# Kernel optimization log

Hardware: AMD Instinct MI355X
Metric: run time of the kernel (lower is better)

## Reference

```python
import jax, jax.numpy as jnp
import numpy as np
from jax import lax

B, T, I, H, L, O = 256, 1024, 64, 128, 2, 1


def setup_inputs() -> dict:
    key = jax.random.key(0)
    ks = jax.random.split(key, 4 * L + 3)
    s = 1.0 / np.sqrt(H)  # PyTorch LSTM init scale
    inp = {"x": jax.random.normal(ks[0], (B, T, I), dtype=jnp.float32)}
    for l in range(L):
        in_dim = I if l == 0 else H
        inp[f"W_ih_{l}"] = jax.random.uniform(ks[1 + 4 * l], (4 * H, in_dim), minval=-s, maxval=s)
        inp[f"W_hh_{l}"] = jax.random.uniform(ks[2 + 4 * l], (4 * H, H), minval=-s, maxval=s)
        inp[f"b_ih_{l}"] = jax.random.uniform(ks[3 + 4 * l], (4 * H,), minval=-s, maxval=s)
        inp[f"b_hh_{l}"] = jax.random.uniform(ks[4 + 4 * l], (4 * H,), minval=-s, maxval=s)
    inp["W_lin"] = jax.random.uniform(ks[-2], (O, H), minval=-s, maxval=s)
    inp["b_lin"] = jax.random.uniform(ks[-1], (O,), minval=-s, maxval=s)
    return inp


def _lstm_layer(x, W_ih, W_hh, b_ih, b_hh):
    # x: [B, T, in] -> hidden states [B, T, H]; PyTorch gate order i, f, g, o
    b = b_ih + b_hh
    # precompute input projections for all timesteps (one big GEMM)
    x_proj = jnp.einsum('bti,gi->btg', x, W_ih) + b  # [B, T, 4H]

    def step(carry, xp_t):
        h, c = carry
        gates = xp_t + h @ W_hh.T  # [B, 4H]
        i, f, g, o = jnp.split(gates, 4, axis=-1)
        c = jax.nn.sigmoid(f) * c + jax.nn.sigmoid(i) * jnp.tanh(g)
        h = jax.nn.sigmoid(o) * jnp.tanh(c)
        return (h, c), h

    h0 = jnp.zeros((x.shape[0], W_hh.shape[1]), x.dtype)
    (_, _), hs = lax.scan(step, (h0, h0), jnp.swapaxes(x_proj, 0, 1))
    return jnp.swapaxes(hs, 0, 1)  # [B, T, H]


def reference(x, W_ih_0, W_hh_0, b_ih_0, b_hh_0, W_ih_1, W_hh_1, b_ih_1, b_hh_1, W_lin, b_lin):
    h = _lstm_layer(x, W_ih_0, W_hh_0, b_ih_0, b_hh_0)
    h = _lstm_layer(h, W_ih_1, W_hh_1, b_ih_1, b_hh_1)
    return h[:, -1] @ W_lin.T + b_lin  # [B, O]
```

## Files before the change

kernel.cpp:

```cpp
#include <hip/hip_runtime.h>


typedef __attribute__((ext_vector_type(4))) float f32x4;
typedef _Float16 f16x8 __attribute__((ext_vector_type(8)));
typedef short s16x8 __attribute__((ext_vector_type(8)));

#define NB    256
#define TSEQ  1024
#define II    64
#define HH    128
#define G4    512
#define TC    16
#define NCH   (TSEQ/TC)
#define SCL   0.0009765625f
#define SCLI  1024.f

#define F_WHH0  0
#define F_WHH1  8192
#define F_WIH1  16384
#define F_WIH0  24576
#define F_TOTAL 28672

#define H0G_OFF   458752ULL
#define H0G_WORDS (256ULL*1024ULL*128ULL)
#define FLAG_OFF  (H0G_OFF + H0G_WORDS*4ULL)
#define WS_NEEDED (FLAG_OFF + 1024ULL)

#define KEEP4I(v) asm volatile("" : "+v"((v).x), "+v"((v).y), "+v"((v).z), "+v"((v).w))

__device__ __forceinline__ float tanh_f(float x){
    float ax = fabsf(x);
    float e  = __expf(2.f*ax);
    float t  = 1.f - 2.f*__builtin_amdgcn_rcpf(e + 1.f);
    return copysignf(t, x);
}
__device__ __forceinline__ f32x4 mfma16(int4 a, f16x8 b, f32x4 c){
    return __builtin_amdgcn_mfma_f32_16x16x32_f16(
        __builtin_bit_cast(f16x8, a), b, c, 0, 0, 0);
}
__device__ __forceinline__ f16x8 ldb(const _Float16* p){
    return __builtin_bit_cast(f16x8, *(const int4*)p);
}
__device__ __forceinline__ void unpack8(int4 v0, int4 v1, f16x8& bh, f16x8& bl){
    s16x8 hb, lb;
    hb[0]=(short)v0.x; lb[0]=(short)(((unsigned)v0.x)>>16);
    hb[1]=(short)v0.y; lb[1]=(short)(((unsigned)v0.y)>>16);
    hb[2]=(short)v0.z; lb[2]=(short)(((unsigned)v0.z)>>16);
    hb[3]=(short)v0.w; lb[3]=(short)(((unsigned)v0.w)>>16);
    hb[4]=(short)v1.x; lb[4]=(short)(((unsigned)v1.x)>>16);
    hb[5]=(short)v1.y; lb[5]=(short)(((unsigned)v1.y)>>16);
    hb[6]=(short)v1.z; lb[6]=(short)(((unsigned)v1.z)>>16);
    hb[7]=(short)v1.w; lb[7]=(short)(((unsigned)v1.w)>>16);
    bh = __builtin_bit_cast(f16x8, hb);
    bl = __builtin_bit_cast(f16x8, lb);
}

__global__ void pack_w(const float* __restrict__ Wih0, const float* __restrict__ Whh0,
                       const float* __restrict__ Wih1, const float* __restrict__ Whh1,
                       int4* __restrict__ ws)
{
    int fid = blockIdx.x * 256 + threadIdx.x;
    if (fid >= F_TOTAL) return;
    const float* src; int nks; int rb;
    if (fid < F_WHH1)      { src = Whh0; nks = 4; rb = fid; }
    else if (fid < F_WIH1) { src = Whh1; nks = 4; rb = fid - F_WHH1; }
    else if (fid < F_WIH0) { src = Wih1; nks = 4; rb = fid - F_WIH1; }
    else                   { src = Wih0; nks = 2; rb = fid - F_WIH0; }
    int lane = rb & 63;
    int rem  = rb >> 6;
    int s    = rem % nks;
    int t    = (rem / nks) & 3;
    int w    = rem / (nks * 4);
    int row  = t * 128 + w * 16 + (lane & 15);
    int K    = nks * 32;
    int k0   = s * 32 + (lane >> 4) * 8;
    const float* p = src + (size_t)row * K + k0;
    unsigned short us[8];
    #pragma unroll
    for (int j = 0; j < 8; ++j)
        us[j] = __builtin_bit_cast(unsigned short, (_Float16)p[j]);
    int4 o;
    o.x = (int)((unsigned)us[0] | ((unsigned)us[1] << 16));
    o.y = (int)((unsigned)us[2] | ((unsigned)us[3] << 16));
    o.z = (int)((unsigned)us[4] | ((unsigned)us[5] << 16));
    o.w = (int)((unsigned)us[6] | ((unsigned)us[7] << 16));
    ws[fid] = o;
}

struct LaneCtx {
    int gsel, usel, u, xpr, base;
    bool writer, is_g, odd;
    int lk;
};

template<bool PING>
__device__ __forceinline__ void serial_steps(
    const LaneCtx& L, const int4 (&Ahi)[4][4],
    float (*xp)[G4],
    _Float16* hh_rd_base, _Float16* hl_rd_base, int rd_stride,
    _Float16* hh_wr_base, _Float16* hl_wr_base, int wr_stride,
    float* h1f, float& c)
{
    #pragma unroll 1
    for (int t = 0; t < TC; ++t){
        int rs = PING ? (t & 1) : t;
        int wsl = PING ? ((t+1) & 1) : (t+1);
        const _Float16* bp = L.odd ? (hl_rd_base + rs*rd_stride)
                                   : (hh_rd_base + rs*rd_stride);
        float xpv = xp[t][L.xpr];
        f32x4 acc[4];
        #pragma unroll
        for (int t4 = 0; t4 < 4; ++t4) acc[t4] = (f32x4){0.f,0.f,0.f,0.f};
        #pragma unroll
        for (int s = 0; s < 4; ++s){
            f16x8 bv = ldb(&bp[s*32 + L.lk*8]);
            #pragma unroll
            for (int t4 = 0; t4 < 4; ++t4) acc[t4] = mfma16(Ahi[t4][s], bv, acc[t4]);
        }
        f32x4 ps;
        {
            f32x4 p01 = (L.gsel & 1) ? acc[1] : acc[0];
            f32x4 p23 = (L.gsel & 1) ? acc[3] : acc[2];
            ps = (L.gsel & 2) ? p23 : p01;
        }
        float own, oth;
        {
            float a01 = (L.usel & 1) ? ps[1] : ps[0];
            float a23 = (L.usel & 1) ? ps[3] : ps[2];
            own = (L.usel & 2) ? a23 : a01;
            float b01 = (L.usel & 1) ? ps[0] : ps[1];
            float b23 = (L.usel & 1) ? ps[2] : ps[3];
            oth = (L.usel & 2) ? b23 : b01;
        }
        float recv = __shfl_xor(oth, 1);
        float pre  = (L.odd ? (recv + SCL*own) : (own + SCL*recv)) + xpv;
        float z    = tanh_f(L.is_g ? pre : 0.5f*pre);
        float y    = L.is_g ? z : 0.5f*z + 0.5f;
        float gi = __shfl(y, L.base);
        float gf = __shfl(y, L.base | 4);
        float gg = __shfl(y, L.base | 8);
        float go = __shfl(y, L.base | 12);
        c = gf*c + gi*gg;
        float h = go * tanh_f(c);
        _Float16 hf = (_Float16)h;
        _Float16 hl = (_Float16)((h - (float)hf) * SCLI);
        if (L.writer){
            (hh_wr_base + wsl*wr_stride)[L.u] = hf;
            (hl_wr_base + wsl*wr_stride)[L.u] = hl;
            if (h1f) h1f[L.u] = h;
        }
        __syncthreads();
    }
}

__global__ __launch_bounds__(512, 2)
void lstm_dual(const float* __restrict__ x,
               const float* __restrict__ bih0, const float* __restrict__ bhh0,
               const float* __restrict__ bih1, const float* __restrict__ bhh1,
               const float* __restrict__ Wlin, const float* __restrict__ blin,
               const int4* __restrict__ ws,
               unsigned* __restrict__ h0g,
               int* __restrict__ prod,
               float* __restrict__ out)
{
    const int tid  = threadIdx.x;
    const int lane = tid & 63;
    const int w    = tid >> 6;
    const int lm   = lane & 15;
    const int lk   = lane >> 4;

    LaneCtx L;
    L.gsel = lm >> 2;  L.usel = lm & 3;  L.lk = lk;
    L.u    = w*16 + lk*4 + L.usel;
    L.xpr  = L.gsel*128 + w*16 + lk*4 + L.usel;
    L.base = lane & 0x33;
    L.writer = (L.gsel == 0);
    L.is_g   = (L.gsel == 2);
    L.odd    = (lane & 1);

    __shared__ __align__(16) char smem[46624];
    float (*xp)[G4] = (float(*)[G4])smem;

    if (blockIdx.x < NB) {
        const int row = blockIdx.x;
        _Float16 (*h0_hi)[136] = (_Float16(*)[136])(smem + 32768);
        _Float16 (*h0_lo)[136] = (_Float16(*)[136])(smem + 37392);
        _Float16 (*xc_hi)[72]  = (_Float16(*)[72]) (smem + 42016);
        _Float16 (*xc_lo)[72]  = (_Float16(*)[72]) (smem + 44320);

        if (tid < HH){ h0_hi[0][tid] = (_Float16)0.f; h0_lo[0][tid] = (_Float16)0.f; }
        float c0 = 0.f;
        const float* xb = x + (size_t)row * TSEQ * II;
        __syncthreads();

        #pragma unroll 1
        for (int ch = 0; ch < NCH; ++ch){
            {
                int i0 = tid, i1 = tid + 512;
                float v0 = xb[(size_t)ch*TC*II + i0];
                float v1 = xb[(size_t)ch*TC*II + i1];
                _Float16 a0 = (_Float16)v0, a1 = (_Float16)v1;
                xc_hi[i0>>6][i0&63] = a0; xc_lo[i0>>6][i0&63] = (_Float16)((v0-(float)a0)*SCLI);
                xc_hi[i1>>6][i1&63] = a1; xc_lo[i1>>6][i1&63] = (_Float16)((v1-(float)a1)*SCLI);
            }
            if (ch > 0 && tid < HH){
                h0_hi[0][tid] = h0_hi[TC][tid];
                h0_lo[0][tid] = h0_lo[TC][tid];
            }
            __syncthreads();

            {
                f32x4 acc[4], accL[4];
                #pragma unroll
                for (int t4 = 0; t4 < 4; ++t4){
                    acc[t4]  = (f32x4){0.f,0.f,0.f,0.f};
                    accL[t4] = (f32x4){0.f,0.f,0.f,0.f};
                }
                #pragma unroll
                for (int s = 0; s < 2; ++s){
                    f16x8 bh = ldb(&xc_hi[lm][s*32 + lk*8]);
                    f16x8 bl = ldb(&xc_lo[lm][s*32 + lk*8]);
                    int4 ah[4];
                    #pragma unroll
                    for (int t4 = 0; t4 < 4; ++t4)
                        ah[t4] = ws[F_WIH0 + (((w*4 + t4)*2 + s) << 6) + lane];
                    #pragma unroll
                    for (int t4 = 0; t4 < 4; ++t4) acc[t4]  = mfma16(ah[t4], bh, acc[t4]);
                    #pragma unroll
                    for (int t4 = 0; t4 < 4; ++t4) accL[t4] = mfma16(ah[t4], bl, accL[t4]);
                }
                #pragma unroll
                for (int t4 = 0; t4 < 4; ++t4){
                    int rowb = t4*128 + w*16 + lk*4;
                    f32x4 bs = *(const f32x4*)(bih0+rowb) + *(const f32x4*)(bhh0+rowb);
                    *(f32x4*)&xp[lm][rowb] = acc[t4] + accL[t4]*SCL + bs;
                }
            }
            __syncthreads();

            int4 Ahi[4][4];
            #pragma unroll
            for (int t4 = 0; t4 < 4; ++t4)
                #pragma unroll
                for (int s = 0; s < 4; ++s)
                    Ahi[t4][s] = ws[F_WHH0 + (((w*4 + t4)*4 + s) << 6) + lane];
            #pragma unroll
            for (int t4 = 0; t4 < 4; ++t4)
                #pragma unroll
                for (int s = 0; s < 4; ++s) KEEP4I(Ahi[t4][s]);

            serial_steps<false>(L, Ahi, xp,
                                &h0_hi[0][0], &h0_lo[0][0], 136,
                                &h0_hi[0][0], &h0_lo[0][0], 136,
                                nullptr, c0);

            {
                size_t gbase = ((size_t)row*TSEQ + (size_t)ch*TC)*HH;
                #pragma unroll
                for (int k = 0; k < 4; ++k){
                    int idx = tid + 512*k;
                    int t = idx >> 7, u = idx & 127;
                    unsigned ph = (unsigned)__builtin_bit_cast(unsigned short, h0_hi[t+1][u]);
                    unsigned pl = (unsigned)__builtin_bit_cast(unsigned short, h0_lo[t+1][u]);
                    h0g[gbase + idx] = ph | (pl << 16);
                }
            }
            __syncthreads();
            if (tid == 0)
                __hip_atomic_store(&prod[row], ch+1, __ATOMIC_RELEASE,
                                   __HIP_MEMORY_SCOPE_AGENT);
        }
    } else {
        const int row = blockIdx.x - NB;
        _Float16 (*h1_hi)[HH] = (_Float16(*)[HH])(smem + 32768);
        _Float16 (*h1_lo)[HH] = (_Float16(*)[HH])(smem + 33280);
        float*    h1f         = (float*)(smem + 33792);

        if (tid < HH){ h1_hi[0][tid] = (_Float16)0.f; h1_lo[0][tid] = (_Float16)0.f;
                       h1f[tid] = 0.f; }
        float c1 = 0.f;
        __syncthreads();

        #pragma unroll 1
        for (int ch = 0; ch < NCH; ++ch){
            {
                int v = __hip_atomic_load(&prod[row], __ATOMIC_RELAXED,
                                          __HIP_MEMORY_SCOPE_AGENT);
                while (v < ch+1){
                    __builtin_amdgcn_s_sleep(8);
                    v = __hip_atomic_load(&prod[row], __ATOMIC_RELAXED,
                                          __HIP_MEMORY_SCOPE_AGENT);
                }
                (void)__hip_atomic_load(&prod[row], __ATOMIC_ACQUIRE,
                                        __HIP_MEMORY_SCOPE_AGENT);
            }
            {
                f32x4 acc[4], accL[4];
                #pragma unroll
                for (int t4 = 0; t4 < 4; ++t4){
                    acc[t4]  = (f32x4){0.f,0.f,0.f,0.f};
                    accL[t4] = (f32x4){0.f,0.f,0.f,0.f};
                }
                size_t gbase = ((size_t)row*TSEQ + (size_t)ch*TC + lm)*HH;
                #pragma unroll
                for (int s = 0; s < 4; ++s){
                    const int4* gp = (const int4*)(h0g + gbase + s*32 + lk*8);
                    int4 v0 = gp[0], v1 = gp[1];
                    f16x8 bh, bl;
                    unpack8(v0, v1, bh, bl);
                    int4 ah[4];
                    #pragma unroll
                    for (int t4 = 0; t4 < 4; ++t4)
                        ah[t4] = ws[F_WIH1 + (((w*4 + t4)*4 + s) << 6) + lane];
                    #pragma unroll
                    for (int t4 = 0; t4 < 4; ++t4) acc[t4]  = mfma16(ah[t4], bh, acc[t4]);
                    #pragma unroll
                    for (int t4 = 0; t4 < 4; ++t4) accL[t4] = mfma16(ah[t4], bl, accL[t4]);
                }
                #pragma unroll
                for (int t4 = 0; t4 < 4; ++t4){
                    int rowb = t4*128 + w*16 + lk*4;
                    f32x4 bs = *(const f32x4*)(bih1+rowb) + *(const f32x4*)(bhh1+rowb);
                    *(f32x4*)&xp[lm][rowb] = acc[t4] + accL[t4]*SCL + bs;
                }
            }
            __syncthreads();

            int4 Ahi[4][4];
            #pragma unroll
            for (int t4 = 0; t4 < 4; ++t4)
                #pragma unroll
                for (int s = 0; s < 4; ++s)
                    Ahi[t4][s] = ws[F_WHH1 + (((w*4 + t4)*4 + s) << 6) + lane];
            #pragma unroll
            for (int t4 = 0; t4 < 4; ++t4)
                #pragma unroll
                for (int s = 0; s < 4; ++s) KEEP4I(Ahi[t4][s]);

            serial_steps<true>(L, Ahi, xp,
                               &h1_hi[0][0], &h1_lo[0][0], HH,
                               &h1_hi[0][0], &h1_lo[0][0], HH,
                               h1f, c1);
        }

        if (tid < 64){
            float s = h1f[tid]*Wlin[tid] + h1f[tid+64]*Wlin[tid+64];
            #pragma unroll
            for (int off = 32; off; off >>= 1) s += __shfl_down(s, off);
            if (tid == 0) out[row] = s + blin[0];
        }
    }
}

extern "C" void kernel_launch(void* const* d_in, const int* in_sizes, int n_in,
                              void* d_out, int out_size, void* d_ws, size_t ws_size,
                              hipStream_t stream)
{
    const float* x    = (const float*)d_in[0];
    const float* Wih0 = (const float*)d_in[1];
    const float* Whh0 = (const float*)d_in[2];
    const float* bih0 = (const float*)d_in[3];
    const float* bhh0 = (const float*)d_in[4];
    const float* Wih1 = (const float*)d_in[5];
    const float* Whh1 = (const float*)d_in[6];
    const float* bih1 = (const float*)d_in[7];
    const float* bhh1 = (const float*)d_in[8];
    const float* Wlin = (const float*)d_in[9];
    const float* blin = (const float*)d_in[10];

    if (ws_size < WS_NEEDED) return;

    char* wsb = (char*)d_ws;
    int4*     ws   = (int4*)wsb;
    unsigned* h0g  = (unsigned*)(wsb + H0G_OFF);
    int*      prod = (int*)(wsb + FLAG_OFF);

    (void)hipMemsetAsync(prod, 0, 1024, stream);
    hipLaunchKernelGGL(pack_w, dim3(F_TOTAL/256), dim3(256), 0, stream,
                       Wih0, Whh0, Wih1, Whh1, ws);
    hipLaunchKernelGGL(lstm_dual, dim3(2*NB), dim3(512), 0, stream,
                       x, bih0, bhh0, bih1, bhh1, Wlin, blin,
                       ws, h0g, prod, (float*)d_out);
}
```

Before: 1.692 ms.

## Fuse both LSTM layers into one 1024-thread block with a skewed chunk pipeline

Replaces the two cooperating 512-thread blocks, which passed layer-0 hidden states through a global buffer guarded by atomic flags, with a single 1024-thread block per batch row. Waves 0-7 run layer 0 on chunk ch while waves 8-15 run layer 1 on chunk ch-1, reading h0 straight from shared memory. This removes the global h0 round trip, the spin-wait polling and the workspace memset. In exchange, every timestep now needs a barrier across all 16 waves. The kernel is forced to 128 VGPRs and one block per CU, which risks register spills and lower occupancy.

```diff
diff --git a/kernel.cpp b/kernel.cpp
--- a/kernel.cpp
+++ b/kernel.cpp
@@ -3,7 +3,6 @@
 
 typedef __attribute__((ext_vector_type(4))) float f32x4;
 typedef _Float16 f16x8 __attribute__((ext_vector_type(8)));
-typedef short s16x8 __attribute__((ext_vector_type(8)));
 
 #define NB    256
 #define TSEQ  1024
@@ -21,11 +20,6 @@
 #define F_WIH0  24576
 #define F_TOTAL 28672
 
-#define H0G_OFF   458752ULL
-#define H0G_WORDS (256ULL*1024ULL*128ULL)
-#define FLAG_OFF  (H0G_OFF + H0G_WORDS*4ULL)
-#define WS_NEEDED (FLAG_OFF + 1024ULL)
-
 #define KEEP4I(v) asm volatile("" : "+v"((v).x), "+v"((v).y), "+v"((v).z), "+v"((v).w))
 
 __device__ __forceinline__ float tanh_f(float x){
@@ -40,19 +34,6 @@
 }
 __device__ __forceinline__ f16x8 ldb(const _Float16* p){
     return __builtin_bit_cast(f16x8, *(const int4*)p);
-}
-__device__ __forceinline__ void unpack8(int4 v0, int4 v1, f16x8& bh, f16x8& bl){
-    s16x8 hb, lb;
-    hb[0]=(short)v0.x; lb[0]=(short)(((unsigned)v0.x)>>16);
-    hb[1]=(short)v0.y; lb[1]=(short)(((unsigned)v0.y)>>16);
-    hb[2]=(short)v0.z; lb[2]=(short)(((unsigned)v0.z)>>16);
-    hb[3]=(short)v0.w; lb[3]=(short)(((unsigned)v0.w)>>16);
-    hb[4]=(short)v1.x; lb[4]=(short)(((unsigned)v1.x)>>16);
-    hb[5]=(short)v1.y; lb[5]=(short)(((unsigned)v1.y)>>16);
-    hb[6]=(short)v1.z; lb[6]=(short)(((unsigned)v1.z)>>16);
-    hb[7]=(short)v1.w; lb[7]=(short)(((unsigned)v1.w)>>16);
-    bh = __builtin_bit_cast(f16x8, hb);
-    bl = __builtin_bit_cast(f16x8, lb);
 }
 
 __global__ void pack_w(const float* __restrict__ Wih0, const float* __restrict__ Whh0,
@@ -93,262 +74,218 @@
     int lk;
 };
 
-template<bool PING>
-__device__ __forceinline__ void serial_steps(
+__device__ __forceinline__ void step_body(
     const LaneCtx& L, const int4 (&Ahi)[4][4],
-    float (*xp)[G4],
-    _Float16* hh_rd_base, _Float16* hl_rd_base, int rd_stride,
-    _Float16* hh_wr_base, _Float16* hl_wr_base, int wr_stride,
+    const float* xpt,
+    const _Float16* hh_rd, const _Float16* hl_rd,
+    _Float16* hh_wr, _Float16* hl_wr,
     float* h1f, float& c)
 {
-    #pragma unroll 1
-    for (int t = 0; t < TC; ++t){
-        int rs = PING ? (t & 1) : t;
-        int wsl = PING ? ((t+1) & 1) : (t+1);
-        const _Float16* bp = L.odd ? (hl_rd_base + rs*rd_stride)
-                                   : (hh_rd_base + rs*rd_stride);
-        float xpv = xp[t][L.xpr];
-        f32x4 acc[4];
+    const _Float16* bp = L.odd ? hl_rd : hh_rd;
+    float xpv = xpt[L.xpr];
+    f32x4 acc[4];
+    #pragma unroll
+    for (int t4 = 0; t4 < 4; ++t4) acc[t4] = (f32x4){0.f,0.f,0.f,0.f};
+    #pragma unroll
+    for (int s = 0; s < 4; ++s){
+        f16x8 bv = ldb(&bp[s*32 + L.lk*8]);
         #pragma unroll
-        for (int t4 = 0; t4 < 4; ++t4) acc[t4] = (f32x4){0.f,0.f,0.f,0.f};
-        #pragma unroll
-        for (int s = 0; s < 4; ++s){
-            f16x8 bv = ldb(&bp[s*32 + L.lk*8]);
-            #pragma unroll
-            for (int t4 = 0; t4 < 4; ++t4) acc[t4] = mfma16(Ahi[t4][s], bv, acc[t4]);
-        }
-        f32x4 ps;
-        {
-            f32x4 p01 = (L.gsel & 1) ? acc[1] : acc[0];
-            f32x4 p23 = (L.gsel & 1) ? acc[3] : acc[2];
-            ps = (L.gsel & 2) ? p23 : p01;
-        }
-        float own, oth;
-        {
-            float a01 = (L.usel & 1) ? ps[1] : ps[0];
-            float a23 = (L.usel & 1) ? ps[3] : ps[2];
-            own = (L.usel & 2) ? a23 : a01;
-            float b01 = (L.usel & 1) ? ps[0] : ps[1];
-            float b23 = (L.usel & 1) ? ps[2] : ps[3];
-            oth = (L.usel & 2) ? b23 : b01;
-        }
-        float recv = __shfl_xor(oth, 1);
-        float pre  = (L.odd ? (recv + SCL*own) : (own + SCL*recv)) + xpv;
-        float z    = tanh_f(L.is_g ? pre : 0.5f*pre);
-        float y    = L.is_g ? z : 0.5f*z + 0.5f;
-        float gi = __shfl(y, L.base);
-        float gf = __shfl(y, L.base | 4);
-        float gg = __shfl(y, L.base | 8);
-        float go = __shfl(y, L.base | 12);
-        c = gf*c + gi*gg;
-        float h = go * tanh_f(c);
-        _Float16 hf = (_Float16)h;
-        _Float16 hl = (_Float16)((h - (float)hf) * SCLI);
-        if (L.writer){
-            (hh_wr_base + wsl*wr_stride)[L.u] = hf;
-            (hl_wr_base + wsl*wr_stride)[L.u] = hl;
-            if (h1f) h1f[L.u] = h;
-        }
-        __syncthreads();
-    }
-}
-
-__global__ __launch_bounds__(512, 2)
-void lstm_dual(const float* __restrict__ x,
-               const float* __restrict__ bih0, const float* __restrict__ bhh0,
-               const float* __restrict__ bih1, const float* __restrict__ bhh1,
-               const float* __restrict__ Wlin, const float* __restrict__ blin,
-               const int4* __restrict__ ws,
-               unsigned* __restrict__ h0g,
-               int* __restrict__ prod,
-               float* __restrict__ out)
+        for (int t4 = 0; t4 < 4; ++t4) acc[t4] = mfma16(Ahi[t4][s], bv, acc[t4]);
+    }
+    f32x4 ps;
+    {
+        f32x4 p01 = (L.gsel & 1) ? acc[1] : acc[0];
+        f32x4 p23 = (L.gsel & 1) ? acc[3] : acc[2];
+        ps = (L.gsel & 2) ? p23 : p01;
+    }
+    float own, oth;
+    {
+        float a01 = (L.usel & 1) ? ps[1] : ps[0];
+        float a23 = (L.usel & 1) ? ps[3] : ps[2];
+        own = (L.usel & 2) ? a23 : a01;
+        float b01 = (L.usel & 1) ? ps[0] : ps[1];
+        float b23 = (L.usel & 1) ? ps[2] : ps[3];
+        oth = (L.usel & 2) ? b23 : b01;
+    }
+    float recv = __shfl_xor(oth, 1);
+    float pre  = (L.odd ? (recv + SCL*own) : (own + SCL*recv)) + xpv;
+    float z    = tanh_f(L.is_g ? pre : 0.5f*pre);
+    float y    = L.is_g ? z : 0.5f*z + 0.5f;
+    float gi = __shfl(y, L.base);
+    float gf = __shfl(y, L.base | 4);
+    float gg = __shfl(y, L.base | 8);
+    float go = __shfl(y, L.base | 12);
+    c = gf*c + gi*gg;
+    float h = go * tanh_f(c);
+    _Float16 hf = (_Float16)h;
+    _Float16 hl = (_Float16)((h - (float)hf) * SCLI);
+    if (L.writer){
+        hh_wr[L.u] = hf;
+        hl_wr[L.u] = hl;
+        if (h1f) h1f[L.u] = h;
+    }
+}
+
+__global__
+__attribute__((amdgpu_flat_work_group_size(1024,1024),
+               amdgpu_waves_per_eu(4,4),
+               amdgpu_num_vgpr(128)))
+void lstm_fused(const float* __restrict__ x,
+                const float* __restrict__ bih0, const float* __restrict__ bhh0,
+                const float* __restrict__ bih1, const float* __restrict__ bhh1,
+                const float* __restrict__ Wlin, const float* __restrict__ blin,
+                const int4* __restrict__ ws,
+                float* __restrict__ out)
 {
+    const int b    = blockIdx.x;
     const int tid  = threadIdx.x;
     const int lane = tid & 63;
     const int w    = tid >> 6;
+    const int eng  = w >> 3;
+    const int we   = w & 7;
     const int lm   = lane & 15;
     const int lk   = lane >> 4;
 
     LaneCtx L;
     L.gsel = lm >> 2;  L.usel = lm & 3;  L.lk = lk;
-    L.u    = w*16 + lk*4 + L.usel;
-    L.xpr  = L.gsel*128 + w*16 + lk*4 + L.usel;
+    L.u    = we*16 + lk*4 + L.usel;
+    L.xpr  = L.gsel*128 + we*16 + lk*4 + L.usel;
     L.base = lane & 0x33;
     L.writer = (L.gsel == 0);
     L.is_g   = (L.gsel == 2);
     L.odd    = (lane & 1);
 
-    __shared__ __align__(16) char smem[46624];
-    float (*xp)[G4] = (float(*)[G4])smem;
-
-    if (blockIdx.x < NB) {
-        const int row = blockIdx.x;
-        _Float16 (*h0_hi)[136] = (_Float16(*)[136])(smem + 32768);
-        _Float16 (*h0_lo)[136] = (_Float16(*)[136])(smem + 37392);
-        _Float16 (*xc_hi)[72]  = (_Float16(*)[72]) (smem + 42016);
-        _Float16 (*xc_lo)[72]  = (_Float16(*)[72]) (smem + 44320);
-
-        if (tid < HH){ h0_hi[0][tid] = (_Float16)0.f; h0_lo[0][tid] = (_Float16)0.f; }
-        float c0 = 0.f;
-        const float* xb = x + (size_t)row * TSEQ * II;
-        __syncthreads();
-
-        #pragma unroll 1
-        for (int ch = 0; ch < NCH; ++ch){
-            {
-                int i0 = tid, i1 = tid + 512;
-                float v0 = xb[(size_t)ch*TC*II + i0];
-                float v1 = xb[(size_t)ch*TC*II + i1];
-                _Float16 a0 = (_Float16)v0, a1 = (_Float16)v1;
-                xc_hi[i0>>6][i0&63] = a0; xc_lo[i0>>6][i0&63] = (_Float16)((v0-(float)a0)*SCLI);
-                xc_hi[i1>>6][i1&63] = a1; xc_lo[i1>>6][i1&63] = (_Float16)((v1-(float)a1)*SCLI);
-            }
+    __shared__ __align__(16) float    xp0[TC][G4];
+    __shared__ __align__(16) float    xp1[TC][G4];
+    __shared__ __align__(16) _Float16 h0_hi[TC+1][136];
+    __shared__ __align__(16) _Float16 h0_lo[TC+1][136];
+    __shared__ __align__(16) _Float16 xc_hi[TC][72];
+    __shared__ __align__(16) _Float16 xc_lo[TC][72];
+    __shared__ __align__(16) _Float16 h1_hi[2][HH];
+    __shared__ __align__(16) _Float16 h1_lo[2][HH];
+    __shared__ __align__(16) float    h1f[HH];
+
+    if (tid < HH){ h0_hi[0][tid] = (_Float16)0.f; h0_lo[0][tid] = (_Float16)0.f; }
+    else if (tid >= 512 && tid < 512 + HH){
+        int u = tid - 512;
+        h1_hi[0][u] = (_Float16)0.f; h1_lo[0][u] = (_Float16)0.f; h1f[u] = 0.f;
+    }
+    float c = 0.f;
+    const float* xb = x + (size_t)b * TSEQ * II;
+    __syncthreads();
+
+    #pragma unroll 1
+    for (int ch = 0; ch <= NCH; ++ch){
+        const bool l0 = (ch < NCH);
+        const bool l1 = (ch > 0);
+
+        if (eng == 0 && l0){
+            int i0 = tid, i1 = tid + 512;
+            float v0 = xb[(size_t)ch*TC*II + i0];
+            float v1 = xb[(size_t)ch*TC*II + i1];
+            _Float16 a0 = (_Float16)v0, a1 = (_Float16)v1;
+            xc_hi[i0>>6][i0&63] = a0; xc_lo[i0>>6][i0&63] = (_Float16)((v0-(float)a0)*SCLI);
+            xc_hi[i1>>6][i1&63] = a1; xc_lo[i1>>6][i1&63] = (_Float16)((v1-(float)a1)*SCLI);
             if (ch > 0 && tid < HH){
                 h0_hi[0][tid] = h0_hi[TC][tid];
                 h0_lo[0][tid] = h0_lo[TC][tid];
             }
+        }
+        __syncthreads();
+
+        if (eng == 0 && l0){
+            f32x4 acc[4], accL[4];
+            #pragma unroll
+            for (int t4 = 0; t4 < 4; ++t4){
+                acc[t4]  = (f32x4){0.f,0.f,0.f,0.f};
+                accL[t4] = (f32x4){0.f,0.f,0.f,0.f};
+            }
+            #pragma unroll
+            for (int s = 0; s < 2; ++s){
+                f16x8 bh = ldb(&xc_hi[lm][s*32 + lk*8]);
+                f16x8 bl = ldb(&xc_lo[lm][s*32 + lk*8]);
+                int4 ah[4];
+                #pragma unroll
+                for (int t4 = 0; t4 < 4; ++t4)
+                    ah[t4] = ws[F_WIH0 + (((we*4 + t4)*2 + s) << 6) + lane];
+                #pragma unroll
+                for (int t4 = 0; t4 < 4; ++t4) acc[t4]  = mfma16(ah[t4], bh, acc[t4]);
+                #pragma unroll
+                for (int t4 = 0; t4 < 4; ++t4) accL[t4] = mfma16(ah[t4], bl, accL[t4]);
+            }
+            #pragma unroll
+            for (int t4 = 0; t4 < 4; ++t4){
+                int rowb = t4*128 + we*16 + lk*4;
+                f32x4 bs = *(const f32x4*)(bih0+rowb) + *(const f32x4*)(bhh0+rowb);
+                *(f32x4*)&xp0[lm][rowb] = acc[t4] + accL[t4]*SCL + bs;
+            }
+        } else if (eng == 1 && l1){
+            f32x4 acc[4], accL[4];
+            #pragma unroll
+            for (int t4 = 0; t4 < 4; ++t4){
+                acc[t4]  = (f32x4){0.f,0.f,0.f,0.f};
+                accL[t4] = (f32x4){0.f,0.f,0.f,0.f};
+            }
+            #pragma unroll
+            for (int s = 0; s < 4; ++s){
+                f16x8 bh = ldb(&h0_hi[lm + 1][s*32 + lk*8]);
+                f16x8 bl = ldb(&h0_lo[lm + 1][s*32 + lk*8]);
+                int4 ah[4];
+                #pragma unroll
+                for (int t4 = 0; t4 < 4; ++t4)
+                    ah[t4] = ws[F_WIH1 + (((we*4 + t4)*4 + s) << 6) + lane];
+                #pragma unroll
+                for (int t4 = 0; t4 < 4; ++t4) acc[t4]  = mfma16(ah[t4], bh, acc[t4]);
+                #pragma unroll
+                for (int t4 = 0; t4 < 4; ++t4) accL[t4] = mfma16(ah[t4], bl, accL[t4]);
+            }
+            #pragma unroll
+            for (int t4 = 0; t4 < 4; ++t4){
+                int rowb = t4*128 + we*16 + lk*4;
+                f32x4 bs = *(const f32x4*)(bih1+rowb) + *(const f32x4*)(bhh1+rowb);
+                *(f32x4*)&xp1[lm][rowb] = acc[t4] + accL[t4]*SCL + bs;
+            }
+        }
+        __syncthreads();
+
+        int4 Ahi[4][4];
+        {
+            const int F = eng ? F_WHH1 : F_WHH0;
+            #pragma unroll
+            for (int t4 = 0; t4 < 4; ++t4)
+                #pragma unroll
+                for (int s = 0; s < 4; ++s)
+                    Ahi[t4][s] = ws[F + (((we*4 + t4)*4 + s) << 6) + lane];
+            #pragma unroll
+            for (int t4 = 0; t4 < 4; ++t4)
+                #pragma unroll
+                for (int s = 0; s < 4; ++s) KEEP4I(Ahi[t4][s]);
+        }
+
+        #pragma unroll 1
+        for (int t = 0; t < TC; ++t){
+            if (eng == 0){
+                if (l0)
+                    step_body(L, Ahi, &xp0[t][0],
+                              &h0_hi[t][0], &h0_lo[t][0],
+                              &h0_hi[t+1][0], &h0_lo[t+1][0],
+                              nullptr, c);
+            } else {
+                if (l1)
+                    step_body(L, Ahi, &xp1[t][0],
+                              &h1_hi[t&1][0], &h1_lo[t&1][0],
+                              &h1_hi[(t+1)&1][0], &h1_lo[(t+1)&1][0],
+                              h1f, c);
+            }
             __syncthreads();
-
-            {
-                f32x4 acc[4], accL[4];
-                #pragma unroll
-                for (int t4 = 0; t4 < 4; ++t4){
-                    acc[t4]  = (f32x4){0.f,0.f,0.f,0.f};
-                    accL[t4] = (f32x4){0.f,0.f,0.f,0.f};
-                }
-                #pragma unroll
-                for (int s = 0; s < 2; ++s){
-                    f16x8 bh = ldb(&xc_hi[lm][s*32 + lk*8]);
-                    f16x8 bl = ldb(&xc_lo[lm][s*32 + lk*8]);
-                    int4 ah[4];
-                    #pragma unroll
-                    for (int t4 = 0; t4 < 4; ++t4)
-                        ah[t4] = ws[F_WIH0 + (((w*4 + t4)*2 + s) << 6) + lane];
-                    #pragma unroll
-                    for (int t4 = 0; t4 < 4; ++t4) acc[t4]  = mfma16(ah[t4], bh, acc[t4]);
-                    #pragma unroll
-                    for (int t4 = 0; t4 < 4; ++t4) accL[t4] = mfma16(ah[t4], bl, accL[t4]);
-                }
-                #pragma unroll
-                for (int t4 = 0; t4 < 4; ++t4){
-                    int rowb = t4*128 + w*16 + lk*4;
-                    f32x4 bs = *(const f32x4*)(bih0+rowb) + *(const f32x4*)(bhh0+rowb);
-                    *(f32x4*)&xp[lm][rowb] = acc[t4] + accL[t4]*SCL + bs;
-                }
-            }
-            __syncthreads();
-
-            int4 Ahi[4][4];
-            #pragma unroll
-            for (int t4 = 0; t4 < 4; ++t4)
-                #pragma unroll
-                for (int s = 0; s < 4; ++s)
-                    Ahi[t4][s] = ws[F_WHH0 + (((w*4 + t4)*4 + s) << 6) + lane];
-            #pragma unroll
-            for (int t4 = 0; t4 < 4; ++t4)
-                #pragma unroll
-                for (int s = 0; s < 4; ++s) KEEP4I(Ahi[t4][s]);
-
-            serial_steps<false>(L, Ahi, xp,
-                                &h0_hi[0][0], &h0_lo[0][0], 136,
-                                &h0_hi[0][0], &h0_lo[0][0], 136,
-                                nullptr, c0);
-
-            {
-                size_t gbase = ((size_t)row*TSEQ + (size_t)ch*TC)*HH;
-                #pragma unroll
-                for (int k = 0; k < 4; ++k){
-                    int idx = tid + 512*k;
-                    int t = idx >> 7, u = idx & 127;
-                    unsigned ph = (unsigned)__builtin_bit_cast(unsigned short, h0_hi[t+1][u]);
-                    unsigned pl = (unsigned)__builtin_bit_cast(unsigned short, h0_lo[t+1][u]);
-                    h0g[gbase + idx] = ph | (pl << 16);
-                }
-            }
-            __syncthreads();
-            if (tid == 0)
-                __hip_atomic_store(&prod[row], ch+1, __ATOMIC_RELEASE,
-                                   __HIP_MEMORY_SCOPE_AGENT);
         }
-    } else {
-        const int row = blockIdx.x - NB;
-        _Float16 (*h1_hi)[HH] = (_Float16(*)[HH])(smem + 32768);
-        _Float16 (*h1_lo)[HH] = (_Float16(*)[HH])(smem + 33280);
-        float*    h1f         = (float*)(smem + 33792);
-
-        if (tid < HH){ h1_hi[0][tid] = (_Float16)0.f; h1_lo[0][tid] = (_Float16)0.f;
-                       h1f[tid] = 0.f; }
-        float c1 = 0.f;
-        __syncthreads();
-
-        #pragma unroll 1
-        for (int ch = 0; ch < NCH; ++ch){
-            {
-                int v = __hip_atomic_load(&prod[row], __ATOMIC_RELAXED,
-                                          __HIP_MEMORY_SCOPE_AGENT);
-                while (v < ch+1){
-                    __builtin_amdgcn_s_sleep(8);
-                    v = __hip_atomic_load(&prod[row], __ATOMIC_RELAXED,
-                                          __HIP_MEMORY_SCOPE_AGENT);
-                }
-                (void)__hip_atomic_load(&prod[row], __ATOMIC_ACQUIRE,
-                                        __HIP_MEMORY_SCOPE_AGENT);
-            }
-            {
-                f32x4 acc[4], accL[4];
-                #pragma unroll
-                for (int t4 = 0; t4 < 4; ++t4){
-                    acc[t4]  = (f32x4){0.f,0.f,0.f,0.f};
-                    accL[t4] = (f32x4){0.f,0.f,0.f,0.f};
-                }
-                size_t gbase = ((size_t)row*TSEQ + (size_t)ch*TC + lm)*HH;
-                #pragma unroll
-                for (int s = 0; s < 4; ++s){
-                    const int4* gp = (const int4*)(h0g + gbase + s*32 + lk*8);
-                    int4 v0 = gp[0], v1 = gp[1];
-                    f16x8 bh, bl;
-                    unpack8(v0, v1, bh, bl);
-                    int4 ah[4];
-                    #pragma unroll
-                    for (int t4 = 0; t4 < 4; ++t4)
-                        ah[t4] = ws[F_WIH1 + (((w*4 + t4)*4 + s) << 6) + lane];
-                    #pragma unroll
-                    for (int t4 = 0; t4 < 4; ++t4) acc[t4]  = mfma16(ah[t4], bh, acc[t4]);
-                    #pragma unroll
-                    for (int t4 = 0; t4 < 4; ++t4) accL[t4] = mfma16(ah[t4], bl, accL[t4]);
-                }
-                #pragma unroll
-                for (int t4 = 0; t4 < 4; ++t4){
-                    int rowb = t4*128 + w*16 + lk*4;
-                    f32x4 bs = *(const f32x4*)(bih1+rowb) + *(const f32x4*)(bhh1+rowb);
-                    *(f32x4*)&xp[lm][rowb] = acc[t4] + accL[t4]*SCL + bs;
-                }
-            }
-            __syncthreads();
-
-            int4 Ahi[4][4];
-            #pragma unroll
-            for (int t4 = 0; t4 < 4; ++t4)
-                #pragma unroll
-                for (int s = 0; s < 4; ++s)
-                    Ahi[t4][s] = ws[F_WHH1 + (((w*4 + t4)*4 + s) << 6) + lane];
-            #pragma unroll
-            for (int t4 = 0; t4 < 4; ++t4)
-                #pragma unroll
-                for (int s = 0; s < 4; ++s) KEEP4I(Ahi[t4][s]);
-
-            serial_steps<true>(L, Ahi, xp,
-                               &h1_hi[0][0], &h1_lo[0][0], HH,
-                               &h1_hi[0][0], &h1_lo[0][0], HH,
-                               h1f, c1);
-        }
-
-        if (tid < 64){
-            float s = h1f[tid]*Wlin[tid] + h1f[tid+64]*Wlin[tid+64];
-            #pragma unroll
-            for (int off = 32; off; off >>= 1) s += __shfl_down(s, off);
-            if (tid == 0) out[row] = s + blin[0];
-        }
+    }
+
+    if (tid < 64){
+        float s = h1f[tid]*Wlin[tid] + h1f[tid+64]*Wlin[tid+64];
+        #pragma unroll
+        for (int off = 32; off; off >>= 1) s += __shfl_down(s, off);
+        if (tid == 0) out[b] = s + blin[0];
     }
 }
 
@@ -368,17 +305,12 @@
     const float* Wlin = (const float*)d_in[9];
     const float* blin = (const float*)d_in[10];
 
-    if (ws_size < WS_NEEDED) return;
-
-    char* wsb = (char*)d_ws;
-    int4*     ws   = (int4*)wsb;
-    unsigned* h0g  = (unsigned*)(wsb + H0G_OFF);
-    int*      prod = (int*)(wsb + FLAG_OFF);
-
-    (void)hipMemsetAsync(prod, 0, 1024, stream);
+    if (ws_size < (size_t)F_TOTAL * 16) return;
+
+    int4* ws = (int4*)d_ws;
     hipLaunchKernelGGL(pack_w, dim3(F_TOTAL/256), dim3(256), 0, stream,
                        Wih0, Whh0, Wih1, Whh1, ws);
-    hipLaunchKernelGGL(lstm_dual, dim3(2*NB), dim3(512), 0, stream,
+    hipLaunchKernelGGL(lstm_fused, dim3(NB), dim3(1024), 0, stream,
                        x, bih0, bhh0, bih1, bhh1, Wlin, blin,
-                       ws, h0g, prod, (float*)d_out);
-}
+                       ws, (float*)d_out);
+}
```

Result: slower. 1.958 ms (+15.8%).
